# Kernel optimization log

Hardware: AMD Instinct MI355X
Metric: run time of the kernel (lower is better)

## Reference

```python
import jax, jax.numpy as jnp
import numpy as np


def _bilinear(x, py, px):
    # x: [B,C,H,W]; py,px: [B,K,Ho,Wo] fractional sample coords (zero pad outside)
    B, C, H, W = x.shape
    K, Ho, Wo = py.shape[1], py.shape[2], py.shape[3]
    xf = x.reshape(B, C, H * W)
    y0 = jnp.floor(py)
    x0 = jnp.floor(px)

    def gather(yi, xi):
        valid = (yi >= 0) & (yi <= H - 1) & (xi >= 0) & (xi <= W - 1)
        yc = jnp.clip(yi, 0, H - 1).astype(jnp.int32)
        xc = jnp.clip(xi, 0, W - 1).astype(jnp.int32)
        idx = (yc * W + xc).reshape(B, 1, -1)  # [B,1,K*Ho*Wo]
        v = jnp.take_along_axis(xf, idx, axis=2)  # [B,C,K*Ho*Wo]
        return v * valid.reshape(B, 1, -1)

    wy1 = (py - y0).reshape(B, 1, -1)
    wx1 = (px - x0).reshape(B, 1, -1)
    wy0 = 1.0 - wy1
    wx0 = 1.0 - wx1
    v = (gather(y0, x0) * (wy0 * wx0)
         + gather(y0, x0 + 1) * (wy0 * wx1)
         + gather(y0 + 1, x0) * (wy1 * wx0)
         + gather(y0 + 1, x0 + 1) * (wy1 * wx1))
    return v.reshape(B, C, K, Ho, Wo)


def _deform_merge(x, w_off, b_off, w_def, gamma, beta):
    B, C, H, W = x.shape
    Co = w_def.shape[0]
    K, stride = 4, 2  # 2x2 kernel
    Ho, Wo = H // 2, W // 2
    # offset-predicting conv (same k/s/p as deform conv): [B, 2K, Ho, Wo]
    off = jax.lax.conv_general_dilated(x, w_off, (stride, stride), 'VALID')
    off = off + b_off[None, :, None, None]
    off = off.reshape(B, K, 2, Ho, Wo)  # (dy, dx) per kernel tap
    ky = jnp.arange(K) // 2
    kx = jnp.arange(K) % 2
    base_y = (jnp.arange(Ho) * stride)[None, None, :, None] + ky[None, :, None, None]
    base_x = (jnp.arange(Wo) * stride)[None, None, None, :] + kx[None, :, None, None]
    py = base_y.astype(x.dtype) + off[:, :, 0]
    px = base_x.astype(x.dtype) + off[:, :, 1]
    sampled = _bilinear(x, py, px)  # [B,C,K,Ho,Wo]
    y = jnp.einsum('bckhw,ock->bohw', sampled, w_def.reshape(Co, C, K))
    # BatchNorm2d (training-mode batch stats, eps=1e-5) + exact GELU
    mu = y.mean(axis=(0, 2, 3), keepdims=True)
    var = y.var(axis=(0, 2, 3), keepdims=True)
    yn = (y - mu) * jax.lax.rsqrt(var + 1e-5)
    yn = yn * gamma[None, :, None, None] + beta[None, :, None, None]
    yg = jax.nn.gelu(yn, approximate=False)
    return yg.reshape(B, Co, Ho * Wo).transpose(0, 2, 1)  # [B, L/4, Co]


def setup_inputs() -> dict:
    key = jax.random.key(0)
    k0, k1, k2 = jax.random.split(key, 3)
    B, C, H, W, Co = 16, 96, 112, 112, 192
    x = jax.random.normal(k0, (B, C, H, W), jnp.float32)
    # conv_offset: 2*kh*kw = 8 output channels (zero-init in mmcv; small random here)
    w_off = jax.random.normal(k1, (8, C, 2, 2), jnp.float32) * 0.01
    b_off = jnp.zeros((8,), jnp.float32)
    w_def = jax.random.normal(k2, (Co, C, 2, 2), jnp.float32) * (1.0 / np.sqrt(C * 4))
    gamma = jnp.ones((Co,), jnp.float32)
    beta = jnp.zeros((Co,), jnp.float32)
    return {"x": x, "h": H, "w": W, "w_off": w_off, "b_off": b_off,
            "w_def": w_def, "gamma": gamma, "beta": beta}


def reference(x, h, w, w_off, b_off, w_def, gamma, beta):
    assert x.shape[2] == h and x.shape[3] == w
    return _deform_merge(x, w_off, b_off, w_def, gamma, beta)
```

## Files before the change

### kernel.cpp

```cpp
#include <hip/hip_runtime.h>
#include <math.h>

#define BB 16
#define CC 96
#define HH 112
#define WW 112
#define HO 56
#define WO 56
#define LL (HO*WO)
#define CO 192
#define CKD 384
#define NPIX (BB*LL)

#define TPX 28
#define CHK 8
#define NCHUNK 12
#define WROWS 4
#define WCOLS 64
#define WSTRIDE 260
#define APAD 40
#define OSTRIDE 228

#define WS_SSUM  16
#define WS_SSQS  208
#define WS_B_OFF 4096
#define B_ELEMS  73728
#define WS_SOFF_OFF 299008
#define SOFF_BYTES (BB*HO*WO*8*4)

typedef short bf16x8 __attribute__((ext_vector_type(8)));
typedef float f32x4  __attribute__((ext_vector_type(4)));

__device__ __forceinline__ void split8(const float4 a0, const float4 a1,
                                       bf16x8& hi, bf16x8& lo)
{
    float f[8] = {a0.x, a0.y, a0.z, a0.w, a1.x, a1.y, a1.z, a1.w};
    #pragma unroll
    for (int j = 0; j < 8; ++j) {
        unsigned bits = __float_as_uint(f[j]);
        float fh = __uint_as_float(bits & 0xFFFF0000u);
        float fl = f[j] - fh;
        hi[j] = (short)(bits >> 16);
        lo[j] = (short)(__float_as_uint(fl) >> 16);
    }
}

__global__ void k_zero(float* __restrict__ ws) {
    int t = threadIdx.x;
    if (t < 384) ws[WS_SSUM + t] = 0.f;
}

__global__ void k_prep(const float* __restrict__ w_def,
                       unsigned short* __restrict__ bhi,
                       unsigned short* __restrict__ blo,
                       float* __restrict__ ws)
{
    if (blockIdx.x == 0 && threadIdx.x < 384) ws[WS_SSUM + threadIdx.x] = 0.f;
    int t = blockIdx.x * 256 + threadIdx.x;
    if (t >= 12 * 12 * 64) return;
    int ln  = t & 63;
    int ks  = (t >> 6) % 12;
    int ntg = t / (64 * 12);
    int n  = ntg * 16 + (ln & 15);
    int k0 = ks * 32 + (ln >> 4) * 8;
    const float* wp = w_def + (size_t)n * CKD + k0;
    #pragma unroll
    for (int j = 0; j < 8; ++j) {
        float f = wp[j];
        unsigned bits = __float_as_uint(f);
        float fh = __uint_as_float(bits & 0xFFFF0000u);
        float fl = f - fh;
        bhi[t * 8 + j] = (unsigned short)(bits >> 16);
        blo[t * 8 + j] = (unsigned short)(__float_as_uint(fl) >> 16);
    }
}

__global__ __launch_bounds__(512) void k_off(
    const float* __restrict__ x, const float* __restrict__ w_off,
    const float* __restrict__ b_off, float* __restrict__ soff_all)
{
    __shared__ float win[CHK * OSTRIDE];
    const int t  = threadIdx.x;
    const int oy = blockIdx.x;
    const int b  = blockIdx.y;
    const int iy = oy * 2;
    const int pix = t >> 3, och = t & 7;
    float dacc = 0.f;
    for (int ch = 0; ch < NCHUNK; ++ch) {
        __syncthreads();
        if (t < 448) {
            int c = t / 56, u = t % 56;
            int r = u / 28, q = u % 28;
            const float* src = x + (((size_t)(b*CC + ch*CHK + c)*HH) + iy + r)*WW + q*4;
            *(float4*)&win[c*OSTRIDE + r*112 + q*4] = *(const float4*)src;
        }
        __syncthreads();
        if (t < 448) {
            const float* wb = w_off + (size_t)och * (CC*4) + ch*CHK*4;
            #pragma unroll
            for (int c = 0; c < CHK; ++c) {
                float2 t0 = *(const float2*)&win[c*OSTRIDE + 2*pix];
                float2 t1 = *(const float2*)&win[c*OSTRIDE + 112 + 2*pix];
                float4 a = *(const float4*)(wb + c*4);
                dacc += t0.x*a.x + t0.y*a.y + t1.x*a.z + t1.y*a.w;
            }
        }
    }
    if (t < 448)
        soff_all[((size_t)(b*HO + oy)*WO)*8 + t] = dacc + b_off[och];
}

__global__ __launch_bounds__(512, 8) void k_main8(
    const float* __restrict__ x,
    const unsigned short* __restrict__ bhi, const unsigned short* __restrict__ blo,
    const float* __restrict__ soff_all,
    float* __restrict__ yout, float* __restrict__ ws)
{
    __shared__ float win[CHK * WSTRIDE];
    __shared__ unsigned short smAh[32 * APAD];
    __shared__ unsigned short smAl[32 * APAD];
    __shared__ float soff[TPX * 8];

    const int tid = threadIdx.x;
    const int b  = blockIdx.y;
    const int bx = blockIdx.x;
    const int oy  = bx >> 1;
    const int ox0 = (bx & 1) * TPX;
    const int iy  = oy * 2;
    const int ix0 = ox0 * 2;
    const int ln = tid & 63;
    const int w  = tid >> 6;
    const int wr = w & 1;
    const int wc = w >> 1;
    const int row0 = ln & 15;
    const int kg   = ln >> 4;

    if (tid < 128) {
        int rr = 28 + (tid >> 5), cc = tid & 31;
        smAh[rr*APAD + cc] = 0;
        smAl[rr*APAD + cc] = 0;
    }
    if (tid < 56) {
        const float* sp = soff_all + ((size_t)(b*HO + oy)*WO + ox0)*8;
        *(float4*)&soff[tid*4] = *(const float4*)(sp + tid*4);
    }

    const int cg  = tid & 15;
    const int pr  = tid >> 4;
    const int sr  = pr & 3;
    const int scn = pr >> 2;
    const int skk = tid & 31;
    const int sc  = skk >> 2;
    const int sk  = skk & 3;
    const int sky = sk >> 1, skx = sk & 1;
    const int wr0 = iy - 1, wc0 = ix0 - 4;

    f32x4 acc[3];
    #pragma unroll
    for (int nt = 0; nt < 3; ++nt) acc[nt] = (f32x4){0.f, 0.f, 0.f, 0.f};

    for (int ch = NCHUNK - 1; ch >= 0; --ch) {
        __syncthreads();
        {
            int gr = min(max(wr0 + sr, 0), HH - 1);
            int gc0 = wc0 + cg * 4;
            const float* src = x + (((size_t)(b*CC + ch*CHK + scn)*HH) + gr)*WW;
            float4 v;
            if (gc0 >= 0 && gc0 <= WW - 4) {
                v = *(const float4*)(src + gc0);
            } else {
                v.x = src[min(max(gc0 + 0, 0), WW - 1)];
                v.y = src[min(max(gc0 + 1, 0), WW - 1)];
                v.z = src[min(max(gc0 + 2, 0), WW - 1)];
                v.w = src[min(max(gc0 + 3, 0), WW - 1)];
            }
            *(float4*)&win[scn*WSTRIDE + sr*WCOLS + cg*4] = v;
        }
        __syncthreads();
        {
            const float* xc = x + ((size_t)(b*CC + ch*CHK + sc)*HH)*WW;
            const float* wchan = &win[sc*WSTRIDE];
            #pragma unroll
            for (int j = 0; j < 2; ++j) {
                int pix = (tid >> 5) + 16 * j;
                if (pix < TPX) {
                    float2 so = *(const float2*)&soff[pix*8 + 2*sk];
                    float fy = (float)(iy + sky) + so.x;
                    float fx = (float)(ix0 + 2*pix + skx) + so.y;
                    float y0f = floorf(fy), x0f = floorf(fx);
                    int y0 = (int)y0f, x0 = (int)x0f;
                    float wy1 = fy - y0f, wx1 = fx - x0f;
                    float wy0 = 1.f - wy1, wx0 = 1.f - wx1;
                    int y1 = y0 + 1, x1 = x0 + 1;
                    bool vy0 = (y0 >= 0) && (y0 <= HH - 1);
                    bool vy1 = (y1 >= 0) && (y1 <= HH - 1);
                    bool vx0 = (x0 >= 0) && (x0 <= WW - 1);
                    bool vx1 = (x1 >= 0) && (x1 <= WW - 1);
                    int cy0 = min(max(y0, 0), HH - 1), cy1 = min(max(y1, 0), HH - 1);
                    int cx0 = min(max(x0, 0), WW - 1), cx1 = min(max(x1, 0), WW - 1);
                    float w00 = (vy0 && vx0) ? wy0 * wx0 : 0.f;
                    float w01 = (vy0 && vx1) ? wy0 * wx1 : 0.f;
                    float w10 = (vy1 && vx0) ? wy1 * wx0 : 0.f;
                    float w11 = (vy1 && vx1) ? wy1 * wx1 : 0.f;
                    int ry0 = cy0 - wr0, ry1 = cy1 - wr0;
                    int rx0 = cx0 - wc0, rx1 = cx1 - wc0;
                    bool inw = ((unsigned)ry0 <= (unsigned)(WROWS - 1)) &&
                               ((unsigned)ry1 <= (unsigned)(WROWS - 1)) &&
                               ((unsigned)rx0 <= (unsigned)(WCOLS - 1)) &&
                               ((unsigned)rx1 <= (unsigned)(WCOLS - 1));
                    float v;
                    if (inw) {
                        v = w00 * wchan[ry0*WCOLS + rx0] + w01 * wchan[ry0*WCOLS + rx1]
                          + w10 * wchan[ry1*WCOLS + rx0] + w11 * wchan[ry1*WCOLS + rx1];
                    } else {
                        v = w00 * xc[cy0*WW + cx0] + w01 * xc[cy0*WW + cx1]
                          + w10 * xc[cy1*WW + cx0] + w11 * xc[cy1*WW + cx1];
                    }
                    unsigned u = __float_as_uint(v);
                    float fh = __uint_as_float(u & 0xFFFF0000u);
                    smAh[pix*APAD + skk] = (unsigned short)(u >> 16);
                    smAl[pix*APAD + skk] = (unsigned short)(__float_as_uint(v - fh) >> 16);
                }
            }
        }
        __syncthreads();
        bf16x8 ah = *(const bf16x8*)&smAh[(wr*16 + row0)*APAD + kg*8];
        bf16x8 al = *(const bf16x8*)&smAl[(wr*16 + row0)*APAD + kg*8];
        #pragma unroll
        for (int nt = 0; nt < 3; ++nt) {
            size_t idx = ((size_t)(((wc*3 + nt)*12 + ch)*64) + ln)*8;
            bf16x8 bh = *(const bf16x8*)(bhi + idx);
            bf16x8 bl = *(const bf16x8*)(blo + idx);
            acc[nt] = __builtin_amdgcn_mfma_f32_16x16x32_bf16(ah, bh, acc[nt], 0, 0, 0);
            acc[nt] = __builtin_amdgcn_mfma_f32_16x16x32_bf16(ah, bl, acc[nt], 0, 0, 0);
            acc[nt] = __builtin_amdgcn_mfma_f32_16x16x32_bf16(al, bh, acc[nt], 0, 0, 0);
        }
    }

    #pragma unroll
    for (int nt = 0; nt < 3; ++nt) {
        float s = 0.f, q = 0.f;
        #pragma unroll
        for (int r = 0; r < 4; ++r) {
            float v = acc[nt][r];
            s += v; q += v * v;
        }
        s += __shfl_xor(s, 16); s += __shfl_xor(s, 32);
        q += __shfl_xor(q, 16); q += __shfl_xor(q, 32);
        if (ln < 16) {
            atomicAdd(&ws[WS_SSUM + wc*48 + nt*16 + ln], s);
            atomicAdd(&ws[WS_SSQS + wc*48 + nt*16 + ln], q);
        }
    }
    size_t obase = (size_t)b * LL + (size_t)oy * WO + ox0;
    #pragma unroll
    for (int r = 0; r < 4; ++r) {
        int pp = wr*16 + kg*4 + r;
        if (pp < TPX) {
            float* dst = yout + (obase + pp)*CO + wc*48 + row0;
            dst[0]  = acc[0][r];
            dst[16] = acc[1][r];
            dst[32] = acc[2][r];
        }
    }
}

template<bool PREP>
__device__ __forceinline__ void tile_body(
    const float* __restrict__ x, const float* __restrict__ w_off,
    const float* __restrict__ b_off, const float* __restrict__ w_def,
    const unsigned short* __restrict__ bhi, const unsigned short* __restrict__ blo,
    float* win, unsigned short* smAh, unsigned short* smAl, float* soff,
    int b, int bx, int tid, f32x4 (&acc)[2][3])
{
    const int oy  = bx >> 1;
    const int ox0 = (bx & 1) * TPX;
    const int iy  = oy * 2;
    const int ix0 = ox0 * 2;
    const int ln = tid & 63;
    const int w  = tid >> 6;

    float dacc = 0.f;
    const int cpix = tid >> 3;
    const int coch = tid & 7;
    const int spair = tid / 14;
    const int sq    = tid % 14;
    for (int ch = 0; ch < NCHUNK; ++ch) {
        __syncthreads();
        if (tid < 224) {
            int c = spair >> 1, r = spair & 1;
            const float* src = x + (((size_t)(b*CC + ch*CHK + c)*HH) + iy + r)*WW + ix0 + sq*4;
            *(float4*)&win[(c*2 + r)*56 + sq*4] = *(const float4*)src;
        }
        __syncthreads();
        if (tid < 224) {
            const float* wb = w_off + (size_t)coch*(CC*4) + ch*CHK*4;
            #pragma unroll
            for (int c = 0; c < CHK; ++c) {
                float2 t0 = *(const float2*)&win[(c*2 + 0)*56 + 2*cpix];
                float2 t1 = *(const float2*)&win[(c*2 + 1)*56 + 2*cpix];
                float4 a = *(const float4*)(wb + c*4);
                dacc += t0.x*a.x + t0.y*a.y + t1.x*a.z + t1.y*a.w;
            }
        }
    }
    if (tid < 224) soff[cpix*8 + coch] = dacc + b_off[coch];

    const int row0 = ln & 15;
    const int kg   = ln >> 4;
    const int skk = tid & 31;
    const int sc  = skk >> 2;
    const int sk  = skk & 3;
    const int sky = sk >> 1, skx = sk & 1;
    const int wr0 = iy - 1, wc0 = ix0 - 4;

    for (int ch = NCHUNK - 1; ch >= 0; --ch) {
        __syncthreads();
        #pragma unroll
        for (int j = 0; j < 2; ++j) {
            int li = tid + 256*j;
            int cg = li & 15;
            int pr = li >> 4;
            int r = pr & 3, c = pr >> 2;
            int gr = min(max(wr0 + r, 0), HH - 1);
            int gc0 = wc0 + cg*4;
            const float* src = x + (((size_t)(b*CC + ch*CHK + c)*HH) + gr)*WW;
            float4 v;
            if (gc0 >= 0 && gc0 <= WW - 4) {
                v = *(const float4*)(src + gc0);
            } else {
                v.x = src[min(max(gc0 + 0, 0), WW - 1)];
                v.y = src[min(max(gc0 + 1, 0), WW - 1)];
                v.z = src[min(max(gc0 + 2, 0), WW - 1)];
                v.w = src[min(max(gc0 + 3, 0), WW - 1)];
            }
            *(float4*)&win[c*WSTRIDE + r*WCOLS + cg*4] = v;
        }
        __syncthreads();
        {
            const float* xc = x + ((size_t)(b*CC + ch*CHK + sc)*HH)*WW;
            const float* wchan = &win[sc*WSTRIDE];
            #pragma unroll
            for (int j = 0; j < 4; ++j) {
                if (j < 3 || tid < 128) {
                    int pix = (tid >> 5) + 8*j;
                    float2 so = *(const float2*)&soff[pix*8 + 2*sk];
                    float fy = (float)(iy + sky) + so.x;
                    float fx = (float)(ix0 + 2*pix + skx) + so.y;
                    float y0f = floorf(fy), x0f = floorf(fx);
                    int y0 = (int)y0f, x0 = (int)x0f;
                    float wy1 = fy - y0f, wx1 = fx - x0f;
                    float wy0 = 1.f - wy1, wx0 = 1.f - wx1;
                    int y1 = y0 + 1, x1 = x0 + 1;
                    bool vy0 = (y0 >= 0) && (y0 <= HH - 1);
                    bool vy1 = (y1 >= 0) && (y1 <= HH - 1);
                    bool vx0 = (x0 >= 0) && (x0 <= WW - 1);
                    bool vx1 = (x1 >= 0) && (x1 <= WW - 1);
                    int cy0 = min(max(y0, 0), HH - 1), cy1 = min(max(y1, 0), HH - 1);
                    int cx0 = min(max(x0, 0), WW - 1), cx1 = min(max(x1, 0), WW - 1);
                    float w00 = (vy0 && vx0) ? wy0*wx0 : 0.f;
                    float w01 = (vy0 && vx1) ? wy0*wx1 : 0.f;
                    float w10 = (vy1 && vx0) ? wy1*wx0 : 0.f;
                    float w11 = (vy1 && vx1) ? wy1*wx1 : 0.f;
                    int ry0 = cy0 - wr0, ry1 = cy1 - wr0;
                    int rx0 = cx0 - wc0, rx1 = cx1 - wc0;
                    bool inw = ((unsigned)ry0 <= (unsigned)(WROWS - 1)) &&
                               ((unsigned)ry1 <= (unsigned)(WROWS - 1)) &&
                               ((unsigned)rx0 <= (unsigned)(WCOLS - 1)) &&
                               ((unsigned)rx1 <= (unsigned)(WCOLS - 1));
                    float v;
                    if (inw) {
                        v = w00*wchan[ry0*WCOLS + rx0] + w01*wchan[ry0*WCOLS + rx1]
                          + w10*wchan[ry1*WCOLS + rx0] + w11*wchan[ry1*WCOLS + rx1];
                    } else {
                        v = w00*xc[cy0*WW + cx0] + w01*xc[cy0*WW + cx1]
                          + w10*xc[cy1*WW + cx0] + w11*xc[cy1*WW + cx1];
                    }
                    unsigned u = __float_as_uint(v);
                    float fh = __uint_as_float(u & 0xFFFF0000u);
                    smAh[pix*APAD + skk] = (unsigned short)(u >> 16);
                    smAl[pix*APAD + skk] = (unsigned short)(__float_as_uint(v - fh) >> 16);
                }
            }
        }
        __syncthreads();
        bf16x8 ah[2], al[2];
        #pragma unroll
        for (int mt = 0; mt < 2; ++mt) {
            ah[mt] = *(const bf16x8*)&smAh[(mt*16 + row0)*APAD + kg*8];
            al[mt] = *(const bf16x8*)&smAl[(mt*16 + row0)*APAD + kg*8];
        }
        #pragma unroll
        for (int nt = 0; nt < 3; ++nt) {
            bf16x8 bh, bl;
            if (PREP) {
                size_t idx = ((size_t)(((w*3 + nt)*12 + ch)*64) + ln)*8;
                bh = *(const bf16x8*)(bhi + idx);
                bl = *(const bf16x8*)(blo + idx);
            } else {
                const float* wp = w_def + (size_t)(w*48 + nt*16 + row0)*CKD + ch*32 + kg*8;
                float4 b0 = *(const float4*)wp;
                float4 b1 = *(const float4*)(wp + 4);
                split8(b0, b1, bh, bl);
            }
            #pragma unroll
            for (int mt = 0; mt < 2; ++mt) {
                acc[mt][nt] = __builtin_amdgcn_mfma_f32_16x16x32_bf16(ah[mt], bh, acc[mt][nt], 0, 0, 0);
                acc[mt][nt] = __builtin_amdgcn_mfma_f32_16x16x32_bf16(ah[mt], bl, acc[mt][nt], 0, 0, 0);
                acc[mt][nt] = __builtin_amdgcn_mfma_f32_16x16x32_bf16(al[mt], bh, acc[mt][nt], 0, 0, 0);
            }
        }
    }
}

template<bool PREP>
__global__ __launch_bounds__(256, 4) void k_main_r3(
    const float* __restrict__ x, const float* __restrict__ w_off,
    const float* __restrict__ b_off, const float* __restrict__ w_def,
    const unsigned short* __restrict__ bhi, const unsigned short* __restrict__ blo,
    float* __restrict__ yout, float* __restrict__ ws)
{
    __shared__ float win[CHK * WSTRIDE];
    __shared__ unsigned short smAh[32 * APAD];
    __shared__ unsigned short smAl[32 * APAD];
    __shared__ float soff[TPX * 8];

    const int tid = threadIdx.x;
    const int b  = blockIdx.y;
    const int bx = blockIdx.x;
    const int ln = tid & 63;
    const int w  = tid >> 6;
    const int row0 = ln & 15;
    const int kg   = ln >> 4;

    if (tid < 128) {
        int rr = 28 + (tid >> 5), cc = tid & 31;
        smAh[rr*APAD + cc] = 0;
        smAl[rr*APAD + cc] = 0;
    }

    f32x4 acc[2][3];
    #pragma unroll
    for (int mt = 0; mt < 2; ++mt)
        #pragma unroll
        for (int nt = 0; nt < 3; ++nt)
            acc[mt][nt] = (f32x4){0.f, 0.f, 0.f, 0.f};

    tile_body<PREP>(x, w_off, b_off, w_def, bhi, blo,
                    win, smAh, smAl, soff, b, bx, tid, acc);

    #pragma unroll
    for (int nt = 0; nt < 3; ++nt) {
        float s = 0.f, q = 0.f;
        #pragma unroll
        for (int mt = 0; mt < 2; ++mt)
            #pragma unroll
            for (int r = 0; r < 4; ++r) {
                float v = acc[mt][nt][r];
                s += v; q += v * v;
            }
        s += __shfl_xor(s, 16); s += __shfl_xor(s, 32);
        q += __shfl_xor(q, 16); q += __shfl_xor(q, 32);
        if (ln < 16) {
            atomicAdd(&ws[WS_SSUM + w*48 + nt*16 + ln], s);
            atomicAdd(&ws[WS_SSQS + w*48 + nt*16 + ln], q);
        }
    }
    int oy = bx >> 1, ox0 = (bx & 1)*TPX;
    size_t obase = (size_t)b*LL + (size_t)oy*WO + ox0;
    #pragma unroll
    for (int mt = 0; mt < 2; ++mt)
        #pragma unroll
        for (int r = 0; r < 4; ++r) {
            int pp = mt*16 + kg*4 + r;
            if (pp < TPX) {
                float* dst = yout + (obase + pp)*CO + w*48 + row0;
                dst[0]  = acc[mt][0][r];
                dst[16] = acc[mt][1][r];
                dst[32] = acc[mt][2][r];
            }
        }
}

__global__ __launch_bounds__(256) void k_bn_gelu(
    float* __restrict__ out,
    const float* __restrict__ gamma,
    const float* __restrict__ beta,
    const float* __restrict__ ws)
{
    __shared__ float ssc[CO], ssh[CO];
    int t = threadIdx.x;
    if (t < CO) {
        float n = (float)NPIX;
        float mu = ws[WS_SSUM + t] / n;
        float var = ws[WS_SSQS + t] / n - mu * mu;
        float sc = gamma[t] * rsqrtf(fmaxf(var, 0.f) + 1e-5f);
        ssc[t] = sc;
        ssh[t] = beta[t] - mu * sc;
    }
    __syncthreads();
    long long i4 = ((long long)blockIdx.x * 256 + t) * 4;
    if (i4 >= (long long)NPIX * CO) return;
    int o0 = (int)(i4 % CO);
    float4* p = (float4*)(out + i4);
    float4 v = *p;
    float f[4] = { v.x, v.y, v.z, v.w };
    #pragma unroll
    for (int j = 0; j < 4; ++j) {
        float z = ssc[o0 + j] * f[j] + ssh[o0 + j];
        f[j] = 0.5f * z * (1.f + erff(z * 0.70710678118654752f));
    }
    v.x = f[0]; v.y = f[1]; v.z = f[2]; v.w = f[3];
    *p = v;
}

extern "C" void kernel_launch(void* const* d_in, const int* in_sizes, int n_in,
                              void* d_out, int out_size, void* d_ws, size_t ws_size,
                              hipStream_t stream)
{
    const float *x = nullptr, *w_off = nullptr, *b_off = nullptr;
    const float *w_def = nullptr, *gamma = nullptr, *beta = nullptr;
    for (int i = 0; i < n_in; ++i) {
        int s = in_sizes[i];
        if      (s == 19267584) x     = (const float*)d_in[i];
        else if (s == 3072)     w_off = (const float*)d_in[i];
        else if (s == 8)        b_off = (const float*)d_in[i];
        else if (s == 73728)    w_def = (const float*)d_in[i];
        else if (s == 192) { if (!gamma) gamma = (const float*)d_in[i];
                             else        beta  = (const float*)d_in[i]; }
    }
    if (!x || !w_off || !b_off || !w_def || !gamma || !beta) {
        x = (const float*)d_in[0]; w_off = (const float*)d_in[3];
        b_off = (const float*)d_in[4]; w_def = (const float*)d_in[5];
        gamma = (const float*)d_in[6]; beta = (const float*)d_in[7];
    }

    float* ws = (float*)d_ws;
    float* out = (float*)d_out;

    unsigned short* bhi = (unsigned short*)((char*)d_ws + WS_B_OFF);
    unsigned short* blo = bhi + B_ELEMS;
    float* soff_all = (float*)((char*)d_ws + WS_SOFF_OFF);
    bool big = ws_size >= (size_t)(WS_SOFF_OFF + SOFF_BYTES);

    if (big) {
        k_prep<<<36, 256, 0, stream>>>(w_def, bhi, blo, ws);
        k_off<<<dim3(HO, BB), 512, 0, stream>>>(x, w_off, b_off, soff_all);
        k_main8<<<dim3(112, BB), 512, 0, stream>>>(x, bhi, blo, soff_all, out, ws);
    } else {
        bool prep = ws_size >= (size_t)(WS_B_OFF + 2*B_ELEMS*sizeof(unsigned short));
        if (prep) {
            k_prep<<<36, 256, 0, stream>>>(w_def, bhi, blo, ws);
            k_main_r3<true><<<dim3(112, BB), 256, 0, stream>>>(x, w_off, b_off, w_def, bhi, blo, out, ws);
        } else {
            k_zero<<<1, 384, 0, stream>>>(ws);
            k_main_r3<false><<<dim3(112, BB), 256, 0, stream>>>(x, w_off, b_off, w_def, bhi, blo, out, ws);
        }
    }
    k_bn_gelu<<<dim3((int)(((long long)NPIX*CO/4 + 255) / 256)), 256, 0, stream>>>(out, gamma, beta, ws);
}
```

Baseline: 336.5 us.

## Merge prep and offset kernels, register-prefetch input chunks in offset and main loops

```diff
diff --git a/kernel.cpp b/kernel.cpp
--- a/kernel.cpp
+++ b/kernel.cpp
@@ -75,39 +75,79 @@
     }
 }
 
-__global__ __launch_bounds__(512) void k_off(
+__global__ __launch_bounds__(512) void k_pre(
     const float* __restrict__ x, const float* __restrict__ w_off,
-    const float* __restrict__ b_off, float* __restrict__ soff_all)
+    const float* __restrict__ b_off, const float* __restrict__ w_def,
+    unsigned short* __restrict__ bhi, unsigned short* __restrict__ blo,
+    float* __restrict__ soff_all, float* __restrict__ ws)
 {
     __shared__ float win[CHK * OSTRIDE];
-    const int t  = threadIdx.x;
-    const int oy = blockIdx.x;
-    const int b  = blockIdx.y;
+    const int blk = blockIdx.x;
+    const int tid = threadIdx.x;
+
+    if (blk < 18) {
+        if (blk == 0 && tid < 384) ws[WS_SSUM + tid] = 0.f;
+        int t = blk * 512 + tid;
+        int ln  = t & 63;
+        int ks  = (t >> 6) % 12;
+        int ntg = t / (64 * 12);
+        int n  = ntg * 16 + (ln & 15);
+        int k0 = ks * 32 + (ln >> 4) * 8;
+        const float* wp = w_def + (size_t)n * CKD + k0;
+        #pragma unroll
+        for (int j = 0; j < 8; ++j) {
+            float f = wp[j];
+            unsigned bits = __float_as_uint(f);
+            float fh = __uint_as_float(bits & 0xFFFF0000u);
+            float fl = f - fh;
+            bhi[t * 8 + j] = (unsigned short)(bits >> 16);
+            blo[t * 8 + j] = (unsigned short)(__float_as_uint(fl) >> 16);
+        }
+        return;
+    }
+
+    const int bb = blk - 18;
+    const int oy = bb % HO;
+    const int b  = bb / HO;
     const int iy = oy * 2;
-    const int pix = t >> 3, och = t & 7;
+    const int pix = tid >> 3, och = tid & 7;
+    const int c_s = tid / 56, u_s = tid % 56;
+    const int r_s = u_s / 28, q_s = u_s % 28;
     float dacc = 0.f;
-    for (int ch = 0; ch < NCHUNK; ++ch) {
-        __syncthreads();
-        if (t < 448) {
-            int c = t / 56, u = t % 56;
-            int r = u / 28, q = u % 28;
-            const float* src = x + (((size_t)(b*CC + ch*CHK + c)*HH) + iy + r)*WW + q*4;
-            *(float4*)&win[c*OSTRIDE + r*112 + q*4] = *(const float4*)src;
-        }
-        __syncthreads();
-        if (t < 448) {
-            const float* wb = w_off + (size_t)och * (CC*4) + ch*CHK*4;
-            #pragma unroll
-            for (int c = 0; c < CHK; ++c) {
-                float2 t0 = *(const float2*)&win[c*OSTRIDE + 2*pix];
-                float2 t1 = *(const float2*)&win[c*OSTRIDE + 112 + 2*pix];
-                float4 a = *(const float4*)(wb + c*4);
-                dacc += t0.x*a.x + t0.y*a.y + t1.x*a.z + t1.y*a.w;
-            }
-        }
-    }
-    if (t < 448)
-        soff_all[((size_t)(b*HO + oy)*WO)*8 + t] = dacc + b_off[och];
+
+    float4 v0, v1, v2;
+    #define OFF_LD(CH) (*(const float4*)(x + (((size_t)(b*CC + (CH)*CHK + c_s)*HH) + iy + r_s)*WW + q_s*4))
+    if (tid < 448) { v0 = OFF_LD(0); v1 = OFF_LD(1); v2 = OFF_LD(2); }
+
+    #define OFF_STEP(CH, VB) \
+        __syncthreads(); \
+        if (tid < 448) { \
+            *(float4*)&win[c_s*OSTRIDE + r_s*112 + q_s*4] = VB; \
+            if ((CH) + 3 < NCHUNK) VB = OFF_LD((CH) + 3); \
+        } \
+        __syncthreads(); \
+        if (tid < 448) { \
+            const float* wb = w_off + (size_t)och*(CC*4) + (CH)*CHK*4; \
+            _Pragma("unroll") \
+            for (int c = 0; c < CHK; ++c) { \
+                float2 t0 = *(const float2*)&win[c*OSTRIDE + 2*pix]; \
+                float2 t1 = *(const float2*)&win[c*OSTRIDE + 112 + 2*pix]; \
+                float4 a = *(const float4*)(wb + c*4); \
+                dacc += t0.x*a.x + t0.y*a.y + t1.x*a.z + t1.y*a.w; \
+            } \
+        }
+
+    #pragma unroll
+    for (int g = 0; g < 4; ++g) {
+        OFF_STEP(3*g + 0, v0)
+        OFF_STEP(3*g + 1, v1)
+        OFF_STEP(3*g + 2, v2)
+    }
+    #undef OFF_STEP
+    #undef OFF_LD
+
+    if (tid < 448)
+        soff_all[((size_t)(b*HO + oy)*WO)*8 + tid] = dacc + b_off[och];
 }
 
 __global__ __launch_bounds__(512, 8) void k_main8(
@@ -155,27 +195,32 @@
     const int sky = sk >> 1, skx = sk & 1;
     const int wr0 = iy - 1, wc0 = ix0 - 4;
 
+    auto stage_ld = [&](int ch) -> float4 {
+        int gr = min(max(wr0 + sr, 0), HH - 1);
+        int gc0 = wc0 + cg * 4;
+        const float* src = x + (((size_t)(b*CC + ch*CHK + scn)*HH) + gr)*WW;
+        float4 v;
+        if (gc0 >= 0 && gc0 <= WW - 4) {
+            v = *(const float4*)(src + gc0);
+        } else {
+            v.x = src[min(max(gc0 + 0, 0), WW - 1)];
+            v.y = src[min(max(gc0 + 1, 0), WW - 1)];
+            v.z = src[min(max(gc0 + 2, 0), WW - 1)];
+            v.w = src[min(max(gc0 + 3, 0), WW - 1)];
+        }
+        return v;
+    };
+    float* wdst = &win[scn*WSTRIDE + sr*WCOLS + cg*4];
+
     f32x4 acc[3];
     #pragma unroll
     for (int nt = 0; nt < 3; ++nt) acc[nt] = (f32x4){0.f, 0.f, 0.f, 0.f};
 
+    float4 vst = stage_ld(NCHUNK - 1);
+    *(float4*)wdst = vst;
+    vst = stage_ld(NCHUNK - 2);
+
     for (int ch = NCHUNK - 1; ch >= 0; --ch) {
-        __syncthreads();
-        {
-            int gr = min(max(wr0 + sr, 0), HH - 1);
-            int gc0 = wc0 + cg * 4;
-            const float* src = x + (((size_t)(b*CC + ch*CHK + scn)*HH) + gr)*WW;
-            float4 v;
-            if (gc0 >= 0 && gc0 <= WW - 4) {
-                v = *(const float4*)(src + gc0);
-            } else {
-                v.x = src[min(max(gc0 + 0, 0), WW - 1)];
-                v.y = src[min(max(gc0 + 1, 0), WW - 1)];
-                v.z = src[min(max(gc0 + 2, 0), WW - 1)];
-                v.w = src[min(max(gc0 + 3, 0), WW - 1)];
-            }
-            *(float4*)&win[scn*WSTRIDE + sr*WCOLS + cg*4] = v;
-        }
         __syncthreads();
         {
             const float* xc = x + ((size_t)(b*CC + ch*CHK + sc)*HH)*WW;
@@ -235,6 +280,8 @@
             acc[nt] = __builtin_amdgcn_mfma_f32_16x16x32_bf16(ah, bl, acc[nt], 0, 0, 0);
             acc[nt] = __builtin_amdgcn_mfma_f32_16x16x32_bf16(al, bh, acc[nt], 0, 0, 0);
         }
+        if (ch > 0) *(float4*)wdst = vst;
+        if (ch > 1) vst = stage_ld(ch - 2);
     }
 
     #pragma unroll
@@ -544,8 +591,7 @@
     bool big = ws_size >= (size_t)(WS_SOFF_OFF + SOFF_BYTES);
 
     if (big) {
-        k_prep<<<36, 256, 0, stream>>>(w_def, bhi, blo, ws);
-        k_off<<<dim3(HO, BB), 512, 0, stream>>>(x, w_off, b_off, soff_all);
+        k_pre<<<18 + HO*BB, 512, 0, stream>>>(x, w_off, b_off, w_def, bhi, blo, soff_all, ws);
         k_main8<<<dim3(112, BB), 512, 0, stream>>>(x, bhi, blo, soff_all, out, ws);
     } else {
         bool prep = ws_size >= (size_t)(WS_B_OFF + 2*B_ELEMS*sizeof(unsigned short));
```

Measured after the change: 347.9 us. 3.4% more time.
